# Kernel tuning notes

Hardware: AMD Instinct MI355X
Metric: run time of the kernel (lower is better)

The kernel has to match this reference:

```python
import jax, jax.numpy as jnp
import numpy as np

B, N, D, E, L = 8, 4096, 256, 65536, 1  # graphs, padded nodes, d_model, padded edges, num_layers


def setup_inputs() -> dict:
    key = jax.random.key(0)
    ks = jax.random.split(key, 9)
    x = jax.random.normal(ks[0], (B, N, D), dtype=jnp.float32)
    edge_index = jax.random.randint(ks[1], (B, 2, E), 0, N)
    edge_weight = jax.random.uniform(ks[2], (B, E), dtype=jnp.float32)
    mask = jax.random.randint(ks[3], (B, N), 0, 2).astype(jnp.int32)
    s = 1.0 / np.sqrt(D)
    # GatedGraphConv per-layer linear weight [L, D, D]
    W = jax.random.uniform(ks[4], (L, D, D), jnp.float32, -s, s)
    # GRUCell parameters (r, z, n stacked)
    W_ih = jax.random.uniform(ks[5], (3 * D, D), jnp.float32, -s, s)
    W_hh = jax.random.uniform(ks[6], (3 * D, D), jnp.float32, -s, s)
    b_ih = jax.random.uniform(ks[7], (3 * D,), jnp.float32, -s, s)
    b_hh = jax.random.uniform(ks[8], (3 * D,), jnp.float32, -s, s)
    return {"x": x, "edge_index": edge_index, "edge_weight": edge_weight,
            "mask": mask, "W": W, "W_ih": W_ih, "W_hh": W_hh,
            "b_ih": b_ih, "b_hh": b_hh}


def _gated_graph_conv(x, u, v, ew, W, W_ih, W_hh, b_ih, b_hh):
    """x:[B,N,D]; u,v:[B,E] src/dst indices; ew:[B,E] (already masked)."""
    h = x
    for l in range(L):
        m = jnp.einsum('bnd,de->bne', h, W[l])            # linear transform
        msg = jnp.take_along_axis(m, u[..., None], axis=1) * ew[..., None]  # [B,E,D]
        agg = jax.vmap(lambda ms, vi: jax.ops.segment_sum(ms, vi, num_segments=N))(msg, v)
        # GRUCell(input=agg, hidden=h)
        gi = agg @ W_ih.T + b_ih                          # [B,N,3D]
        gh = h @ W_hh.T + b_hh
        r = jax.nn.sigmoid(gi[..., :D] + gh[..., :D])
        z = jax.nn.sigmoid(gi[..., D:2 * D] + gh[..., D:2 * D])
        n = jnp.tanh(gi[..., 2 * D:] + r * gh[..., 2 * D:])
        h = (1.0 - z) * n + z * h
    return h


def reference(x, edge_index, edge_weight, mask, W, W_ih, W_hh, b_ih, b_hh):
    node_valid = mask > 0                                  # [B,N]
    u = edge_index[:, 0]                                   # source
    v = edge_index[:, 1]                                   # target
    # Drop edges touching invalid nodes: weight -> 0 (equivalent under sum aggr)
    e_valid = jnp.take_along_axis(node_valid, u, axis=1) & jnp.take_along_axis(node_valid, v, axis=1)
    ew = edge_weight * e_valid.astype(edge_weight.dtype)
    h = _gated_graph_conv(x, u, v, ew, W, W_ih, W_hh, b_ih, b_hh)
    # Invalid nodes stay zero (original writes only valid rows of a zeros output)
    return h * node_valid[..., None].astype(h.dtype)
```

## Files before the change

### kernel.cpp

```cpp
#include <hip/hip_runtime.h>
#include <math.h>

#define Bn 8
#define Nn 4096
#define Dn 256
#define En 65536
#define CAP 48

typedef __bf16 bf8 __attribute__((ext_vector_type(8)));
typedef float f4 __attribute__((ext_vector_type(4)));
typedef unsigned short us8 __attribute__((ext_vector_type(8)));

__device__ __forceinline__ float4 ld4(const float* p) { return *(const float4*)p; }

__device__ __forceinline__ unsigned short f2bf(float f) {
    union { float f; unsigned int u; } v; v.f = f;
    unsigned int r = v.u + 0x7fff + ((v.u >> 16) & 1);
    return (unsigned short)(r >> 16);
}
__device__ __forceinline__ float bf2f(unsigned short h) {
    union { unsigned int u; float f; } v; v.u = (unsigned int)h << 16;
    return v.f;
}


__device__ __forceinline__ void stage16c(const unsigned short* __restrict__ gchunk,
                                         int stride, char* ldschunk, int lane) {
    int u = lane >> 3, s = lane & 7;
    int xx = s ^ (u & 7);
    const unsigned short* g = gchunk + (size_t)(2 * u + (xx >> 2)) * stride + (xx & 3) * 8;
    __builtin_amdgcn_global_load_lds((const __attribute__((address_space(1))) void*)g,
                                     (__attribute__((address_space(3))) void*)ldschunk,
                                     16, 0, 0);
}

__device__ __forceinline__ bf8 fragld(const unsigned short* region, int r, int q) {
    int s = (((r & 1) << 2) | q) ^ ((r >> 1) & 7);
    return *(const bf8*)(region + (r >> 1) * 64 + s * 8);
}

__device__ __forceinline__ void ldswrite8(unsigned short* region, int r, int q,
                                          const unsigned short* vals) {
    int s = (((r & 1) << 2) | q) ^ ((r >> 1) & 7);
    *(us8*)(region + (r >> 1) * 64 + s * 8) = *(const us8*)vals;
}


__device__ void rowscan_piece(const int* __restrict__ mask, int* __restrict__ rowidx,
                              int* __restrict__ rowcnt, int* part) {
    int t = threadIdx.x;
    int base = t * 128;
    unsigned long long b0 = 0, b1 = 0;
    int s = 0;
#pragma unroll 8
    for (int i = 0; i < 64; i++) {
        int m = mask[base + i] > 0;
        b0 |= (unsigned long long)m << i; s += m;
    }
#pragma unroll 8
    for (int i = 0; i < 64; i++) {
        int m = mask[base + 64 + i] > 0;
        b1 |= (unsigned long long)m << i; s += m;
    }
    part[t] = s;
    __syncthreads();
    for (int st = 1; st < 256; st <<= 1) {
        int v = (t >= st) ? part[t - st] : 0;
        __syncthreads();
        part[t] += v;
        __syncthreads();
    }
    int run = part[t] - s;
    for (int i = 0; i < 64; i++)
        if ((b0 >> i) & 1) rowidx[run++] = base + i;
    for (int i = 0; i < 64; i++)
        if ((b1 >> i) & 1) rowidx[run++] = base + 64 + i;
    if (t == 255) rowcnt[0] = part[255];
}

__device__ void wf_piece(int wfi, const float* __restrict__ Wih, const float* __restrict__ W,
                         unsigned short* __restrict__ Ball, unsigned short* lds) {
    int t = threadIdx.x, lane = t & 63, w = t >> 6;
    int wr = w >> 1, wc = w & 1, q = lane >> 4, c16 = lane & 15;
    int o0 = (wfi % 6) * 128, d0b = (wfi / 6) * 64;
    f4 acc[4][2];
    f4 zz = {0.f, 0.f, 0.f, 0.f};
#pragma unroll
    for (int rt = 0; rt < 4; rt++)
#pragma unroll
        for (int ct = 0; ct < 2; ct++) acc[rt][ct] = zz;

    int r = t >> 1, half = t & 1;
    for (int k0 = 0; k0 < 256; k0 += 32) {
        const float* pa = Wih + (size_t)(o0 + r) * 256 + k0 + half * 16;
        float4 a0 = ld4(pa), a1 = ld4(pa + 4), a2 = ld4(pa + 8), a3 = ld4(pa + 12);
        float4 b0, b1, b2, b3;
        if (t < 128) {
            const float* pb = W + (size_t)(d0b + r) * 256 + k0 + half * 16;
            b0 = ld4(pb); b1 = ld4(pb + 4); b2 = ld4(pb + 8); b3 = ld4(pb + 12);
        }
        __syncthreads();
        unsigned short tmp[16];
        tmp[0] = f2bf(a0.x); tmp[1] = f2bf(a0.y); tmp[2] = f2bf(a0.z); tmp[3] = f2bf(a0.w);
        tmp[4] = f2bf(a1.x); tmp[5] = f2bf(a1.y); tmp[6] = f2bf(a1.z); tmp[7] = f2bf(a1.w);
        tmp[8] = f2bf(a2.x); tmp[9] = f2bf(a2.y); tmp[10] = f2bf(a2.z); tmp[11] = f2bf(a2.w);
        tmp[12] = f2bf(a3.x); tmp[13] = f2bf(a3.y); tmp[14] = f2bf(a3.z); tmp[15] = f2bf(a3.w);
        ldswrite8(lds, r, half * 2, tmp);
        ldswrite8(lds, r, half * 2 + 1, tmp + 8);
        if (t < 128) {
            unsigned short tb[16];
            tb[0] = f2bf(b0.x); tb[1] = f2bf(b0.y); tb[2] = f2bf(b0.z); tb[3] = f2bf(b0.w);
            tb[4] = f2bf(b1.x); tb[5] = f2bf(b1.y); tb[6] = f2bf(b1.z); tb[7] = f2bf(b1.w);
            tb[8] = f2bf(b2.x); tb[9] = f2bf(b2.y); tb[10] = f2bf(b2.z); tb[11] = f2bf(b2.w);
            tb[12] = f2bf(b3.x); tb[13] = f2bf(b3.y); tb[14] = f2bf(b3.z); tb[15] = f2bf(b3.w);
            ldswrite8(lds + 4096, r, half * 2, tb);
            ldswrite8(lds + 4096, r, half * 2 + 1, tb + 8);
        }
        __syncthreads();
        bf8 a[4];
#pragma unroll
        for (int rt = 0; rt < 4; rt++) a[rt] = fragld(lds, wr * 64 + rt * 16 + c16, q);
#pragma unroll
        for (int ct = 0; ct < 2; ct++) {
            bf8 b = fragld(lds + 4096, wc * 32 + ct * 16 + c16, q);
#pragma unroll
            for (int rt = 0; rt < 4; rt++)
                acc[rt][ct] = __builtin_amdgcn_mfma_f32_16x16x32_bf16(a[rt], b, acc[rt][ct], 0, 0, 0);
        }
    }
#pragma unroll
    for (int ct = 0; ct < 2; ct++) {
        int col = d0b + wc * 32 + ct * 16 + c16;
#pragma unroll
        for (int rt = 0; rt < 4; rt++) {
            int ob = o0 + wr * 64 + rt * 16 + q * 4;
#pragma unroll
            for (int i = 0; i < 4; i++)
                Ball[(size_t)(ob + i) * 512 + col] = f2bf(acc[rt][ct][i]);
        }
    }
}

__global__ __launch_bounds__(256) void setup_kernel(const int* __restrict__ ei,
                                                    const int* __restrict__ mask,
                                                    const float* __restrict__ Wih,
                                                    const float* __restrict__ W,
                                                    const float* __restrict__ Whh,
                                                    const float* __restrict__ ew,
                                                    int* __restrict__ cnt,
                                                    int2* __restrict__ bucket,
                                                    int* __restrict__ rowidx,
                                                    int* __restrict__ rowcnt,
                                                    unsigned short* __restrict__ Ball,
                                                    float* __restrict__ out) {
    __shared__ __align__(16) unsigned short lds[6144];
    int b = blockIdx.x, t = threadIdx.x;
    if (b == 0) {
        rowscan_piece(mask, rowidx, rowcnt, (int*)lds);
        return;
    }
    if (b < 25) {
        wf_piece(b - 1, Wih, W, Ball, lds);
        return;
    }
    if (b < 217) {
        int i = ((b - 25) * 256 + t) * 4;
        float4 wv = ld4(Whh + i);
        int o = i >> 8, d = i & 255;
        ushort4 ov;
        ov.x = f2bf(wv.x); ov.y = f2bf(wv.y); ov.z = f2bf(wv.z); ov.w = f2bf(wv.w);
        *(ushort4*)(Ball + (size_t)o * 512 + 256 + d) = ov;
        return;
    }
    if (b < 2265) {
        int idx = (b - 217) * 256 + t;
        int bb = idx >> 16, e = idx & 65535;
        const int* eb = ei + (size_t)bb * 2 * En;
        int u = eb[e];
        int v = eb[En + e];
        const int* mb = mask + bb * Nn;
        if (mb[u] > 0 && mb[v] > 0) {
            int pos = atomicAdd(&cnt[bb * Nn + v], 1);
            if (pos < CAP) {
                int2 pr;
                pr.x = u;
                pr.y = __float_as_int(ew[(size_t)bb * En + e]);
                bucket[(size_t)(bb * Nn + v) * CAP + pos] = pr;
            }
        }
        return;
    }
    {
        int zb = b - 2265;
        int r = zb * 8 + (t >> 5);
        if (mask[r] > 0) return;
        int col = (t & 31) * 8;
        float4 z = make_float4(0.f, 0.f, 0.f, 0.f);
        *(float4*)(out + (size_t)r * 256 + col) = z;
        *(float4*)(out + (size_t)r * 256 + col + 4) = z;
    }
}


__global__ __launch_bounds__(256) void agg_kernel(const float* __restrict__ x,
                                                  const int* __restrict__ cnt,
                                                  const int2* __restrict__ bucket,
                                                  const int* __restrict__ rowidx,
                                                  const int* __restrict__ rowcnt,
                                                  unsigned short* __restrict__ Ac) {
    int wave = threadIdx.x >> 6, lane = threadIdx.x & 63;
    int i = blockIdx.x * 4 + wave;
    if (i >= rowcnt[0]) return;
    int v = rowidx[i];
    int b = v >> 12, n = v & 4095;
    int m = cnt[b * Nn + n];
    m = m < CAP ? m : CAP;
    const int2* bk = bucket + (size_t)(b * Nn + n) * CAP;
    const float* Xb = x + (size_t)b * Nn * 256;
    float a0 = 0.f, a1 = 0.f, a2 = 0.f, a3 = 0.f;
    for (int j = 0; j < m; j += 8) {
        int u[8]; float wv[8];
#pragma unroll
        for (int k = 0; k < 8; k++) {
            int jj = j + k;
            bool ok = jj < m;
            int2 pr = bk[ok ? jj : 0];
            u[k] = pr.x;
            wv[k] = ok ? __int_as_float(pr.y) : 0.f;
        }
        float4 mv[8];
#pragma unroll
        for (int k = 0; k < 8; k++) mv[k] = ld4(Xb + (size_t)u[k] * 256 + lane * 4);
#pragma unroll
        for (int k = 0; k < 8; k++) {
            a0 += wv[k] * mv[k].x; a1 += wv[k] * mv[k].y;
            a2 += wv[k] * mv[k].z; a3 += wv[k] * mv[k].w;
        }
    }
    ushort4 o;
    o.x = f2bf(a0); o.y = f2bf(a1); o.z = f2bf(a2); o.w = f2bf(a3);
    *(ushort4*)(Ac + (size_t)i * 512 + lane * 4) = o;
    float4 xv = ld4(x + (size_t)v * 256 + lane * 4);
    ushort4 xo;
    xo.x = f2bf(xv.x); xo.y = f2bf(xv.y); xo.z = f2bf(xv.z); xo.w = f2bf(xv.w);
    *(ushort4*)(Ac + (size_t)i * 512 + 256 + lane * 4) = xo;
}


#define GRU_STAGE(kk, bufbase)                                                      \
    {                                                                               \
        if (w < 4) {                                                                \
            _Pragma("unroll") for (int j = 0; j < 3; j++) {                         \
                int c = w * 3 + j;                                                  \
                const unsigned short* src;                                          \
                if (c < 8)                                                          \
                    src = Ac + (size_t)(row0 + c * 16) * 512 + (kk) * 32;           \
                else {                                                              \
                    int g = (c - 8) >> 2, cg = (c - 8) & 3;                         \
                    src = Ball + (size_t)(g * 256 + d0 + cg * 16) * 512 + (kk) * 32;\
                }                                                                   \
                stage16c(src, 512, (char*)(bufbase) + c * 1024, lane);              \
            }                                                                       \
        } else {                                                                    \
            _Pragma("unroll") for (int j = 0; j < 2; j++) {                         \
                int c = 12 + (w - 4) * 2 + j;                                       \
                int g = (c - 8) >> 2, cg = (c - 8) & 3;                             \
                const unsigned short* src =                                         \
                    Ball + (size_t)(g * 256 + d0 + cg * 16) * 512 + (kk) * 32;      \
                stage16c(src, 512, (char*)(bufbase) + c * 1024, lane);              \
            }                                                                       \
        }                                                                           \
    }

#define GRU_COMPUTE(bufbase, ACCM)                                                  \
    {                                                                               \
        const unsigned short* rb = (bufbase);                                       \
        bf8 a0 = fragld(rb + (wr * 2) * 512, c16, q);                               \
        bf8 a1 = fragld(rb + (wr * 2 + 1) * 512, c16, q);                           \
        _Pragma("unroll") for (int ct = 0; ct < 2; ct++) {                          \
            int cg = wc * 2 + ct;                                                   \
            bf8 br = fragld(rb + (8 + cg) * 512, c16, q);                           \
            bf8 bz = fragld(rb + (12 + cg) * 512, c16, q);                          \
            bf8 bm = fragld(rb + (16 + cg) * 512, c16, q);                          \
            acc_r[0][ct] = __builtin_amdgcn_mfma_f32_16x16x32_bf16(a0, br, acc_r[0][ct], 0, 0, 0); \
            acc_r[1][ct] = __builtin_amdgcn_mfma_f32_16x16x32_bf16(a1, br, acc_r[1][ct], 0, 0, 0); \
            acc_z[0][ct] = __builtin_amdgcn_mfma_f32_16x16x32_bf16(a0, bz, acc_z[0][ct], 0, 0, 0); \
            acc_z[1][ct] = __builtin_amdgcn_mfma_f32_16x16x32_bf16(a1, bz, acc_z[1][ct], 0, 0, 0); \
            ACCM[0][ct] = __builtin_amdgcn_mfma_f32_16x16x32_bf16(a0, bm, ACCM[0][ct], 0, 0, 0);   \
            ACCM[1][ct] = __builtin_amdgcn_mfma_f32_16x16x32_bf16(a1, bm, ACCM[1][ct], 0, 0, 0);   \
        }                                                                           \
    }

__global__ __launch_bounds__(512, 4) void gru_kernel(const unsigned short* __restrict__ Ac,
                                                     const unsigned short* __restrict__ Ball,
                                                     const float* __restrict__ bih,
                                                     const float* __restrict__ bhh,
                                                     const int* __restrict__ rowidx,
                                                     const int* __restrict__ rowcnt,
                                                     float* __restrict__ out) {
    __shared__ __align__(16) unsigned short lds[20480];
    const int t = threadIdx.x;
    const int lane = t & 63, w = t >> 6;
    const int wr = w >> 1, wc = w & 1;
    const int q = lane >> 4, c16 = lane & 15;
    const int row0 = blockIdx.x * 128, d0 = blockIdx.y * 64;
    const int cnt = rowcnt[0];
    if (row0 >= cnt) return;

    f4 acc_r[2][2], acc_z[2][2], acc_gn[2][2], acc_hn[2][2];
    f4 zz = {0.f, 0.f, 0.f, 0.f};
#pragma unroll
    for (int rt = 0; rt < 2; rt++)
#pragma unroll
        for (int ct = 0; ct < 2; ct++) {
            acc_r[rt][ct] = zz; acc_z[rt][ct] = zz;
            acc_gn[rt][ct] = zz; acc_hn[rt][ct] = zz;
        }

    unsigned short* buf0 = lds;
    unsigned short* buf1 = lds + 10240;

    GRU_STAGE(0, buf0)
#pragma unroll
    for (int kk = 0; kk < 8; kk++) {
        __syncthreads();
        GRU_STAGE(kk + 1, (kk & 1) ? buf0 : buf1)
        GRU_COMPUTE((kk & 1) ? buf1 : buf0, acc_gn)
    }
#pragma unroll
    for (int kk = 8; kk < 16; kk++) {
        __syncthreads();
        if (kk < 15) GRU_STAGE(kk + 1, (kk & 1) ? buf0 : buf1)
        GRU_COMPUTE((kk & 1) ? buf1 : buf0, acc_hn)
    }

#pragma unroll
    for (int ct = 0; ct < 2; ct++) {
        int dd = d0 + wc * 32 + ct * 16 + c16;
        float b_r = bih[dd] + bhh[dd];
        float b_z = bih[dd + 256] + bhh[dd + 256];
        float b_gn = bih[dd + 512];
        float b_hn = bhh[dd + 512];
#pragma unroll
        for (int rt = 0; rt < 2; rt++) {
            int rbase = row0 + wr * 32 + rt * 16 + q * 4;
#pragma unroll
            for (int i = 0; i < 4; i++) {
                int rc = rbase + i;
                if (rc < cnt) {
                    float sr = acc_r[rt][ct][i] + b_r;
                    float sz = acc_z[rt][ct][i] + b_z;
                    float gn = acc_gn[rt][ct][i] + b_gn;
                    float hn = acc_hn[rt][ct][i] + b_hn;
                    float rg = 1.f / (1.f + __expf(-sr));
                    float zg = 1.f / (1.f + __expf(-sz));
                    float pre = gn + rg * hn;
                    float e2 = __expf(2.f * pre);
                    float ng = 1.f - 2.f / (e2 + 1.f);
                    float xv = bf2f(Ac[(size_t)rc * 512 + 256 + dd]);
                    float h = (1.f - zg) * ng + zg * xv;
                    int v = rowidx[rc];
                    out[(size_t)v * 256 + dd] = h;
                }
            }
        }
    }
}


extern "C" void kernel_launch(void* const* d_in, const int* in_sizes, int n_in,
                              void* d_out, int out_size, void* d_ws, size_t ws_size,
                              hipStream_t stream) {
    const float* x   = (const float*)d_in[0];
    const int*   ei  = (const int*)d_in[1];
    const float* ew  = (const float*)d_in[2];
    const int*   msk = (const int*)d_in[3];
    const float* W   = (const float*)d_in[4];
    const float* Wih = (const float*)d_in[5];
    const float* Whh = (const float*)d_in[6];
    const float* bih = (const float*)d_in[7];
    const float* bhh = (const float*)d_in[8];
    float* out = (float*)d_out;

    char* p = (char*)d_ws;
    unsigned short* Ac   = (unsigned short*)p; p += (size_t)Bn * Nn * 512 * 2;
    unsigned short* Ball = (unsigned short*)p; p += (size_t)768 * 512 * 2;
    int2* bucket = (int2*)p;  p += (size_t)Bn * Nn * CAP * sizeof(int2);
    int* cnt    = (int*)p;    p += (size_t)Bn * Nn * sizeof(int);
    int* rowidx = (int*)p;    p += (size_t)Bn * Nn * sizeof(int);
    int* rowcnt = (int*)p;    p += 128;

    hipMemsetAsync(cnt, 0, (size_t)Bn * Nn * sizeof(int), stream);
    setup_kernel<<<6361, 256, 0, stream>>>(ei, msk, Wih, W, Whh, ew, cnt, bucket,
                                           rowidx, rowcnt, Ball, out);
    agg_kernel<<<(Bn * Nn) / 4, 256, 0, stream>>>(x, cnt, bucket, rowidx, rowcnt, Ac);
    gru_kernel<<<dim3(256, 4), 512, 0, stream>>>(Ac, Ball, bih, bhh, rowidx, rowcnt, out);
}
```

Baseline: 176.9 us.

## Pre-convert x to bf16 for gathers and retile GRU GEMM per wave

```diff
diff --git a/kernel.cpp b/kernel.cpp
--- a/kernel.cpp
+++ b/kernel.cpp
@@ -47,7 +47,8 @@
 
 
 __device__ void rowscan_piece(const int* __restrict__ mask, int* __restrict__ rowidx,
-                              int* __restrict__ rowcnt, int* part) {
+                              int* __restrict__ rowpos, int* __restrict__ rowcnt,
+                              int* part) {
     int t = threadIdx.x;
     int base = t * 128;
     unsigned long long b0 = 0, b1 = 0;
@@ -72,9 +73,9 @@
     }
     int run = part[t] - s;
     for (int i = 0; i < 64; i++)
-        if ((b0 >> i) & 1) rowidx[run++] = base + i;
+        if ((b0 >> i) & 1) { rowidx[run] = base + i; rowpos[base + i] = run; run++; }
     for (int i = 0; i < 64; i++)
-        if ((b1 >> i) & 1) rowidx[run++] = base + 64 + i;
+        if ((b1 >> i) & 1) { rowidx[run] = base + 64 + i; rowpos[base + 64 + i] = run; run++; }
     if (t == 255) rowcnt[0] = part[255];
 }
 
@@ -147,16 +148,18 @@
                                                     const float* __restrict__ W,
                                                     const float* __restrict__ Whh,
                                                     const float* __restrict__ ew,
+                                                    const float* __restrict__ x,
                                                     int* __restrict__ cnt,
                                                     int2* __restrict__ bucket,
                                                     int* __restrict__ rowidx,
+                                                    int* __restrict__ rowpos,
                                                     int* __restrict__ rowcnt,
                                                     unsigned short* __restrict__ Ball,
-                                                    float* __restrict__ out) {
+                                                    unsigned short* __restrict__ xbf) {
     __shared__ __align__(16) unsigned short lds[6144];
     int b = blockIdx.x, t = threadIdx.x;
     if (b == 0) {
-        rowscan_piece(mask, rowidx, rowcnt, (int*)lds);
+        rowscan_piece(mask, rowidx, rowpos, rowcnt, (int*)lds);
         return;
     }
     if (b < 25) {
@@ -191,32 +194,41 @@
         return;
     }
     {
-        int zb = b - 2265;
-        int r = zb * 8 + (t >> 5);
-        if (mask[r] > 0) return;
-        int col = (t & 31) * 8;
-        float4 z = make_float4(0.f, 0.f, 0.f, 0.f);
-        *(float4*)(out + (size_t)r * 256 + col) = z;
-        *(float4*)(out + (size_t)r * 256 + col + 4) = z;
-    }
-}
-
-
-__global__ __launch_bounds__(256) void agg_kernel(const float* __restrict__ x,
+        int idx = (b - 2265) * 256 + t;
+        size_t base = (size_t)idx * 16;
+        float4 v0 = ld4(x + base), v1 = ld4(x + base + 4);
+        float4 v2 = ld4(x + base + 8), v3 = ld4(x + base + 12);
+        us8 o0, o1;
+        o0[0] = f2bf(v0.x); o0[1] = f2bf(v0.y); o0[2] = f2bf(v0.z); o0[3] = f2bf(v0.w);
+        o0[4] = f2bf(v1.x); o0[5] = f2bf(v1.y); o0[6] = f2bf(v1.z); o0[7] = f2bf(v1.w);
+        o1[0] = f2bf(v2.x); o1[1] = f2bf(v2.y); o1[2] = f2bf(v2.z); o1[3] = f2bf(v2.w);
+        o1[4] = f2bf(v3.x); o1[5] = f2bf(v3.y); o1[6] = f2bf(v3.z); o1[7] = f2bf(v3.w);
+        *(us8*)(xbf + base) = o0;
+        *(us8*)(xbf + base + 8) = o1;
+    }
+}
+
+
+__global__ __launch_bounds__(256) void agg_kernel(const unsigned short* __restrict__ xbf,
+                                                  const int* __restrict__ mask,
                                                   const int* __restrict__ cnt,
                                                   const int2* __restrict__ bucket,
-                                                  const int* __restrict__ rowidx,
-                                                  const int* __restrict__ rowcnt,
-                                                  unsigned short* __restrict__ Ac) {
+                                                  const int* __restrict__ rowpos,
+                                                  unsigned short* __restrict__ Ac,
+                                                  float* __restrict__ out) {
     int wave = threadIdx.x >> 6, lane = threadIdx.x & 63;
-    int i = blockIdx.x * 4 + wave;
-    if (i >= rowcnt[0]) return;
-    int v = rowidx[i];
+    int v = blockIdx.x * 4 + wave;
+    if (mask[v] <= 0) {
+        float4 z = make_float4(0.f, 0.f, 0.f, 0.f);
+        *(float4*)(out + (size_t)v * 256 + lane * 4) = z;
+        return;
+    }
     int b = v >> 12, n = v & 4095;
+    int i = rowpos[v];
     int m = cnt[b * Nn + n];
     m = m < CAP ? m : CAP;
     const int2* bk = bucket + (size_t)(b * Nn + n) * CAP;
-    const float* Xb = x + (size_t)b * Nn * 256;
+    const unsigned short* Xb = xbf + ((size_t)(b << 12)) * 256;
     float a0 = 0.f, a1 = 0.f, a2 = 0.f, a3 = 0.f;
     for (int j = 0; j < m; j += 8) {
         int u[8]; float wv[8];
@@ -228,70 +240,25 @@
             u[k] = pr.x;
             wv[k] = ok ? __int_as_float(pr.y) : 0.f;
         }
-        float4 mv[8];
-#pragma unroll
-        for (int k = 0; k < 8; k++) mv[k] = ld4(Xb + (size_t)u[k] * 256 + lane * 4);
+        ushort4 mv[8];
+#pragma unroll
+        for (int k = 0; k < 8; k++)
+            mv[k] = *(const ushort4*)(Xb + (size_t)u[k] * 256 + lane * 4);
 #pragma unroll
         for (int k = 0; k < 8; k++) {
-            a0 += wv[k] * mv[k].x; a1 += wv[k] * mv[k].y;
-            a2 += wv[k] * mv[k].z; a3 += wv[k] * mv[k].w;
+            a0 += wv[k] * bf2f(mv[k].x); a1 += wv[k] * bf2f(mv[k].y);
+            a2 += wv[k] * bf2f(mv[k].z); a3 += wv[k] * bf2f(mv[k].w);
         }
     }
     ushort4 o;
     o.x = f2bf(a0); o.y = f2bf(a1); o.z = f2bf(a2); o.w = f2bf(a3);
     *(ushort4*)(Ac + (size_t)i * 512 + lane * 4) = o;
-    float4 xv = ld4(x + (size_t)v * 256 + lane * 4);
-    ushort4 xo;
-    xo.x = f2bf(xv.x); xo.y = f2bf(xv.y); xo.z = f2bf(xv.z); xo.w = f2bf(xv.w);
-    *(ushort4*)(Ac + (size_t)i * 512 + 256 + lane * 4) = xo;
-}
-
-
-#define GRU_STAGE(kk, bufbase)                                                      \
-    {                                                                               \
-        if (w < 4) {                                                                \
-            _Pragma("unroll") for (int j = 0; j < 3; j++) {                         \
-                int c = w * 3 + j;                                                  \
-                const unsigned short* src;                                          \
-                if (c < 8)                                                          \
-                    src = Ac + (size_t)(row0 + c * 16) * 512 + (kk) * 32;           \
-                else {                                                              \
-                    int g = (c - 8) >> 2, cg = (c - 8) & 3;                         \
-                    src = Ball + (size_t)(g * 256 + d0 + cg * 16) * 512 + (kk) * 32;\
-                }                                                                   \
-                stage16c(src, 512, (char*)(bufbase) + c * 1024, lane);              \
-            }                                                                       \
-        } else {                                                                    \
-            _Pragma("unroll") for (int j = 0; j < 2; j++) {                         \
-                int c = 12 + (w - 4) * 2 + j;                                       \
-                int g = (c - 8) >> 2, cg = (c - 8) & 3;                             \
-                const unsigned short* src =                                         \
-                    Ball + (size_t)(g * 256 + d0 + cg * 16) * 512 + (kk) * 32;      \
-                stage16c(src, 512, (char*)(bufbase) + c * 1024, lane);              \
-            }                                                                       \
-        }                                                                           \
-    }
-
-#define GRU_COMPUTE(bufbase, ACCM)                                                  \
-    {                                                                               \
-        const unsigned short* rb = (bufbase);                                       \
-        bf8 a0 = fragld(rb + (wr * 2) * 512, c16, q);                               \
-        bf8 a1 = fragld(rb + (wr * 2 + 1) * 512, c16, q);                           \
-        _Pragma("unroll") for (int ct = 0; ct < 2; ct++) {                          \
-            int cg = wc * 2 + ct;                                                   \
-            bf8 br = fragld(rb + (8 + cg) * 512, c16, q);                           \
-            bf8 bz = fragld(rb + (12 + cg) * 512, c16, q);                          \
-            bf8 bm = fragld(rb + (16 + cg) * 512, c16, q);                          \
-            acc_r[0][ct] = __builtin_amdgcn_mfma_f32_16x16x32_bf16(a0, br, acc_r[0][ct], 0, 0, 0); \
-            acc_r[1][ct] = __builtin_amdgcn_mfma_f32_16x16x32_bf16(a1, br, acc_r[1][ct], 0, 0, 0); \
-            acc_z[0][ct] = __builtin_amdgcn_mfma_f32_16x16x32_bf16(a0, bz, acc_z[0][ct], 0, 0, 0); \
-            acc_z[1][ct] = __builtin_amdgcn_mfma_f32_16x16x32_bf16(a1, bz, acc_z[1][ct], 0, 0, 0); \
-            ACCM[0][ct] = __builtin_amdgcn_mfma_f32_16x16x32_bf16(a0, bm, ACCM[0][ct], 0, 0, 0);   \
-            ACCM[1][ct] = __builtin_amdgcn_mfma_f32_16x16x32_bf16(a1, bm, ACCM[1][ct], 0, 0, 0);   \
-        }                                                                           \
-    }
-
-__global__ __launch_bounds__(512, 4) void gru_kernel(const unsigned short* __restrict__ Ac,
+    *(ushort4*)(Ac + (size_t)i * 512 + 256 + lane * 4) =
+        *(const ushort4*)(xbf + (size_t)v * 256 + lane * 4);
+}
+
+
+__global__ __launch_bounds__(256, 2) void gru_kernel(const unsigned short* __restrict__ Ac,
                                                      const unsigned short* __restrict__ Ball,
                                                      const float* __restrict__ bih,
                                                      const float* __restrict__ bhh,
@@ -307,51 +274,75 @@
     const int cnt = rowcnt[0];
     if (row0 >= cnt) return;
 
-    f4 acc_r[2][2], acc_z[2][2], acc_gn[2][2], acc_hn[2][2];
+    f4 acc_i[3][4][2], acc_h[3][4][2];
     f4 zz = {0.f, 0.f, 0.f, 0.f};
 #pragma unroll
-    for (int rt = 0; rt < 2; rt++)
+    for (int g = 0; g < 3; g++)
+#pragma unroll
+        for (int rt = 0; rt < 4; rt++)
+#pragma unroll
+            for (int ct = 0; ct < 2; ct++) { acc_i[g][rt][ct] = zz; acc_h[g][rt][ct] = zz; }
+
+    for (int k0 = 0; k0 < 256; k0 += 32) {
+        __syncthreads();
+        stage16c(Ac + (size_t)(row0 + w * 32) * 512 + k0, 512,
+                 (char*)lds + (w * 2) * 1024, lane);
+        stage16c(Ac + (size_t)(row0 + w * 32 + 16) * 512 + k0, 512,
+                 (char*)lds + (w * 2 + 1) * 1024, lane);
+        stage16c(Ac + (size_t)(row0 + w * 32) * 512 + 256 + k0, 512,
+                 (char*)lds + (8 + w * 2) * 1024, lane);
+        stage16c(Ac + (size_t)(row0 + w * 32 + 16) * 512 + 256 + k0, 512,
+                 (char*)lds + (8 + w * 2 + 1) * 1024, lane);
+#pragma unroll
+        for (int j = 0; j < 6; j++) {
+            int id = w * 6 + j;
+            int m = id >> 2, cg = id & 3;
+            int g = m >> 1, h = m & 1;
+            const unsigned short* src =
+                Ball + (size_t)(g * 256 + d0 + cg * 16) * 512 + h * 256 + k0;
+            stage16c(src, 512, (char*)lds + (16 + m * 4 + cg) * 1024, lane);
+        }
+        __syncthreads();
+        bf8 aag[4], ah[4];
+#pragma unroll
+        for (int rt = 0; rt < 4; rt++) {
+            int r = wr * 64 + rt * 16 + c16;
+            aag[rt] = fragld(lds, r, q);
+            ah[rt] = fragld(lds + 4096, r, q);
+        }
 #pragma unroll
         for (int ct = 0; ct < 2; ct++) {
-            acc_r[rt][ct] = zz; acc_z[rt][ct] = zz;
-            acc_gn[rt][ct] = zz; acc_hn[rt][ct] = zz;
-        }
-
-    unsigned short* buf0 = lds;
-    unsigned short* buf1 = lds + 10240;
-
-    GRU_STAGE(0, buf0)
-#pragma unroll
-    for (int kk = 0; kk < 8; kk++) {
-        __syncthreads();
-        GRU_STAGE(kk + 1, (kk & 1) ? buf0 : buf1)
-        GRU_COMPUTE((kk & 1) ? buf1 : buf0, acc_gn)
-    }
-#pragma unroll
-    for (int kk = 8; kk < 16; kk++) {
-        __syncthreads();
-        if (kk < 15) GRU_STAGE(kk + 1, (kk & 1) ? buf0 : buf1)
-        GRU_COMPUTE((kk & 1) ? buf1 : buf0, acc_hn)
-    }
-
+            int cc = wc * 32 + ct * 16 + c16;
+#pragma unroll
+            for (int g = 0; g < 3; g++) {
+                bf8 bi = fragld(lds + 8192 + (g * 2) * 2048, cc, q);
+                bf8 bh = fragld(lds + 8192 + (g * 2 + 1) * 2048, cc, q);
+#pragma unroll
+                for (int rt = 0; rt < 4; rt++) {
+                    acc_i[g][rt][ct] =
+                        __builtin_amdgcn_mfma_f32_16x16x32_bf16(aag[rt], bi, acc_i[g][rt][ct], 0, 0, 0);
+                    acc_h[g][rt][ct] =
+                        __builtin_amdgcn_mfma_f32_16x16x32_bf16(ah[rt], bh, acc_h[g][rt][ct], 0, 0, 0);
+                }
+            }
+        }
+    }
 #pragma unroll
     for (int ct = 0; ct < 2; ct++) {
         int dd = d0 + wc * 32 + ct * 16 + c16;
-        float b_r = bih[dd] + bhh[dd];
-        float b_z = bih[dd + 256] + bhh[dd + 256];
-        float b_gn = bih[dd + 512];
-        float b_hn = bhh[dd + 512];
-#pragma unroll
-        for (int rt = 0; rt < 2; rt++) {
-            int rbase = row0 + wr * 32 + rt * 16 + q * 4;
+        float bir = bih[dd], biz = bih[dd + 256], bin = bih[dd + 512];
+        float bhr = bhh[dd], bhz = bhh[dd + 256], bhn = bhh[dd + 512];
+#pragma unroll
+        for (int rt = 0; rt < 4; rt++) {
+            int rbase = row0 + wr * 64 + rt * 16 + q * 4;
 #pragma unroll
             for (int i = 0; i < 4; i++) {
                 int rc = rbase + i;
                 if (rc < cnt) {
-                    float sr = acc_r[rt][ct][i] + b_r;
-                    float sz = acc_z[rt][ct][i] + b_z;
-                    float gn = acc_gn[rt][ct][i] + b_gn;
-                    float hn = acc_hn[rt][ct][i] + b_hn;
+                    float sr = acc_i[0][rt][ct][i] + bir + acc_h[0][rt][ct][i] + bhr;
+                    float sz = acc_i[1][rt][ct][i] + biz + acc_h[1][rt][ct][i] + bhz;
+                    float gn = acc_i[2][rt][ct][i] + bin;
+                    float hn = acc_h[2][rt][ct][i] + bhn;
                     float rg = 1.f / (1.f + __expf(-sr));
                     float zg = 1.f / (1.f + __expf(-sz));
                     float pre = gn + rg * hn;
@@ -384,15 +375,17 @@
 
     char* p = (char*)d_ws;
     unsigned short* Ac   = (unsigned short*)p; p += (size_t)Bn * Nn * 512 * 2;
+    unsigned short* xbf  = (unsigned short*)p; p += (size_t)Bn * Nn * Dn * 2;
     unsigned short* Ball = (unsigned short*)p; p += (size_t)768 * 512 * 2;
     int2* bucket = (int2*)p;  p += (size_t)Bn * Nn * CAP * sizeof(int2);
     int* cnt    = (int*)p;    p += (size_t)Bn * Nn * sizeof(int);
     int* rowidx = (int*)p;    p += (size_t)Bn * Nn * sizeof(int);
+    int* rowpos = (int*)p;    p += (size_t)Bn * Nn * sizeof(int);
     int* rowcnt = (int*)p;    p += 128;
 
     hipMemsetAsync(cnt, 0, (size_t)Bn * Nn * sizeof(int), stream);
-    setup_kernel<<<6361, 256, 0, stream>>>(ei, msk, Wih, W, Whh, ew, cnt, bucket,
-                                           rowidx, rowcnt, Ball, out);
-    agg_kernel<<<(Bn * Nn) / 4, 256, 0, stream>>>(x, cnt, bucket, rowidx, rowcnt, Ac);
-    gru_kernel<<<dim3(256, 4), 512, 0, stream>>>(Ac, Ball, bih, bhh, rowidx, rowcnt, out);
-}
+    setup_kernel<<<4313, 256, 0, stream>>>(ei, msk, Wih, W, Whh, ew, x, cnt, bucket,
+                                           rowidx, rowpos, rowcnt, Ball, xbf);
+    agg_kernel<<<(Bn * Nn) / 4, 256, 0, stream>>>(xbf, msk, cnt, bucket, rowpos, Ac, out);
+    gru_kernel<<<dim3(256, 4), 256, 0, stream>>>(Ac, Ball, bih, bhh, rowidx, rowcnt, out);
+}
```

New measurement: 182.0 us. 1.03x slower.
